# Performance work log

Hardware: AMD Instinct MI355X
Metric: run time of the kernel (lower is better)

The kernel has to match this reference:

```python
import jax, jax.numpy as jnp
import numpy as np

S, B, E, H, L = 256, 32, 300, 2400, 3


def setup_inputs() -> dict:
    key = jax.random.key(0)
    ks = jax.random.split(key, 8)
    sent = jax.random.normal(ks[0], (S, B, E), dtype=jnp.float32)
    sent_len = jax.random.randint(ks[1], (B,), 1, S + 1, dtype=jnp.int32)
    # QRNN per-layer linear: in_dim -> 3*H (Z, F, O gates), nn.Linear layout [3H, in]
    def lin(k, fan_in):
        s = 1.0 / np.sqrt(fan_in)
        kw, kb = jax.random.split(k)
        W = jax.random.uniform(kw, (3 * H, fan_in), jnp.float32, -s, s)
        b = jax.random.uniform(kb, (3 * H,), jnp.float32, -s, s)
        return W, b
    W1, b1 = lin(ks[2], E)
    W2, b2 = lin(ks[3], H)
    W3, b3 = lin(ks[4], H)
    return {"sent": sent, "sent_len": sent_len,
            "W1": W1, "b1": b1, "W2": W2, "b2": b2, "W3": W3, "b3": b3}


def _qrnn_layer(x, W, b):
    # x: [S, B, D] -> gates [S, B, 3H]
    Y = jnp.einsum('sbd,hd->sbh', x, W) + b
    Z, F, O = jnp.split(Y, 3, axis=-1)
    Z = jnp.tanh(Z)
    F = jax.nn.sigmoid(F)
    O = jax.nn.sigmoid(O)
    c0 = jnp.zeros(Z.shape[1:], Z.dtype)  # [B, H]
    def step(c, zf):
        z, f = zf
        c = f * c + (1.0 - f) * z  # fo-pool elementwise recurrence
        return c, c
    c_last, C = jax.lax.scan(step, c0, (Z, F))
    return O * C, c_last  # hidden seq [S,B,H], final cell [B,H]


def reference(sent, sent_len, W1, b1, W2, b2, W3, b3):
    x = sent
    finals = []
    for (W, b) in ((W1, b1), (W2, b2), (W3, b3)):
        x, c_last = _qrnn_layer(x, W, b)
        finals.append(c_last)
    hidden = jnp.stack(finals, axis=0)  # [L, B, H] == qrnn(...)[1]
    # mean pool as written in the module: sum over dim 0, divide by sent_len
    out = jnp.sum(hidden, axis=0) / sent_len.astype(jnp.float32)[:, None]
    return out  # [B, H]
```

## Files before the change

### kernel.cpp

```cpp
#include <hip/hip_runtime.h>
#include <math.h>
#include <stdint.h>
#include <stddef.h>

#define AS1 __attribute__((address_space(1)))
#define AS3 __attribute__((address_space(3)))

typedef __attribute__((ext_vector_type(8))) __bf16 bf16x8;
typedef __attribute__((ext_vector_type(4))) float f32x4;

#define SQ   256
#define BQ   32
#define EQ   300
#define HQ   2400
#define MQ   (SQ * BQ)
#define N3H  7200
#define N2H  4800
#define KP1  320
#define KP2  2432

__device__ __forceinline__ uint16_t f2bf(float x) {
    uint32_t u = __float_as_uint(x);
    u += 0x7FFFu + ((u >> 16) & 1u);
    return (uint16_t)(u >> 16);
}
__device__ __forceinline__ float bf2f(uint16_t b) {
    return __uint_as_float(((uint32_t)b) << 16);
}
__device__ __forceinline__ float sigm(float x) { return 1.f / (1.f + __expf(-x)); }

__global__ void conv_split(const float* __restrict__ src, uint16_t* __restrict__ hi,
                           uint16_t* __restrict__ lo, int rows, int K, int Kp) {
    int idx = blockIdx.x * 256 + threadIdx.x;
    int total = rows * Kp;
    if (idx >= total) return;
    int r = idx / Kp;
    int k = idx - r * Kp;
    float v = 0.f;
    if (k < K) v = src[(size_t)r * K + k];
    uint16_t h = f2bf(v);
    hi[idx] = h;
    lo[idx] = f2bf(v - bf2f(h));
}

__global__ void zero_pad_X(uint16_t* __restrict__ hi, uint16_t* __restrict__ lo) {
    int idx = blockIdx.x * 256 + threadIdx.x;
    if (idx >= MQ * (KP2 - HQ)) return;
    int r = idx >> 5;
    int c = idx & 31;
    size_t off = (size_t)r * KP2 + HQ + c;
    hi[off] = 0;
    lo[off] = 0;
}

__global__ __launch_bounds__(256, 2) void gemm_split(
    const uint16_t* __restrict__ Ahi, const uint16_t* __restrict__ Alo,
    const uint16_t* __restrict__ Whi, const uint16_t* __restrict__ Wlo,
    float* __restrict__ Y, int Kp, int Ncols, int rowbase)
{
    __shared__ uint16_t lds[4][128][64];
    const int tid  = threadIdx.x;
    const int lane = tid & 63;
    const int wave = tid >> 6;
    const int wm   = wave >> 1;
    const int wn   = wave & 1;
    const int lrow0 = blockIdx.y << 7;
    const int col0  = blockIdx.x << 7;

    const int sr = (wave << 3) + (lane >> 3);
    const int sk = (lane & 7) << 3;
    const int fr = lane & 15;
    const int fk = (lane >> 4) << 3;

    f32x4 acc[4][4];
    f32x4 zero = {0.f, 0.f, 0.f, 0.f};
#pragma unroll
    for (int i = 0; i < 4; ++i)
#pragma unroll
        for (int j = 0; j < 4; ++j) acc[i][j] = zero;

    char* ldsb = (char*)&lds[0][0][0];

    for (int k0 = 0; k0 < Kp; k0 += 64) {
#pragma unroll
        for (int i = 0; i < 4; ++i) {
            const int rr = (i << 5) + sr;
            const size_t ka = (size_t)(rowbase + lrow0 + rr) * Kp + (k0 + sk);
            const int wr = min(col0 + rr, Ncols - 1);
            const size_t kw = (size_t)wr * Kp + (k0 + sk);
            const int lofs = ((i << 5) + (wave << 3)) << 7;
            __builtin_amdgcn_global_load_lds((const AS1 uint32_t*)(Ahi + ka),
                                             (AS3 uint32_t*)(ldsb + lofs),         16, 0, 0);
            __builtin_amdgcn_global_load_lds((const AS1 uint32_t*)(Alo + ka),
                                             (AS3 uint32_t*)(ldsb + 16384 + lofs), 16, 0, 0);
            __builtin_amdgcn_global_load_lds((const AS1 uint32_t*)(Whi + kw),
                                             (AS3 uint32_t*)(ldsb + 32768 + lofs), 16, 0, 0);
            __builtin_amdgcn_global_load_lds((const AS1 uint32_t*)(Wlo + kw),
                                             (AS3 uint32_t*)(ldsb + 49152 + lofs), 16, 0, 0);
        }
        __syncthreads();

#pragma unroll
        for (int kk = 0; kk < 2; ++kk) {
            bf16x8 ah[4], al[4], bh[4], bl[4];
#pragma unroll
            for (int t = 0; t < 4; ++t) {
                ah[t] = *(const bf16x8*)&lds[0][(wm << 6) + (t << 4) + fr][(kk << 5) + fk];
                al[t] = *(const bf16x8*)&lds[1][(wm << 6) + (t << 4) + fr][(kk << 5) + fk];
                bh[t] = *(const bf16x8*)&lds[2][(wn << 6) + (t << 4) + fr][(kk << 5) + fk];
                bl[t] = *(const bf16x8*)&lds[3][(wn << 6) + (t << 4) + fr][(kk << 5) + fk];
            }
#pragma unroll
            for (int mi = 0; mi < 4; ++mi)
#pragma unroll
                for (int ni = 0; ni < 4; ++ni) {
                    acc[mi][ni] = __builtin_amdgcn_mfma_f32_16x16x32_bf16(ah[mi], bh[ni], acc[mi][ni], 0, 0, 0);
                    acc[mi][ni] = __builtin_amdgcn_mfma_f32_16x16x32_bf16(ah[mi], bl[ni], acc[mi][ni], 0, 0, 0);
                    acc[mi][ni] = __builtin_amdgcn_mfma_f32_16x16x32_bf16(al[mi], bh[ni], acc[mi][ni], 0, 0, 0);
                }
        }
        __syncthreads();
    }

    const int orow = (lane >> 4) << 2;
    const int ocol = lane & 15;
#pragma unroll
    for (int mi = 0; mi < 4; ++mi) {
        const int r0 = lrow0 + (wm << 6) + (mi << 4) + orow;
#pragma unroll
        for (int ni = 0; ni < 4; ++ni) {
            const int c = col0 + (wn << 6) + (ni << 4) + ocol;
            if (c < Ncols) {
                float* yp = Y + (size_t)r0 * Ncols + c;
#pragma unroll
                for (int r = 0; r < 4; ++r) yp[(size_t)r * Ncols] = acc[mi][ni][r];
            }
        }
    }
}

template<int MODE>
__global__ void scan_k(const float* __restrict__ Y, const float* __restrict__ bias,
                       uint16_t* __restrict__ hhi, uint16_t* __restrict__ hlo,
                       float* __restrict__ cst, float* __restrict__ fin,
                       float* __restrict__ out, const int* __restrict__ slen,
                       int s0, int Sc)
{
    int idx = blockIdx.x * 256 + threadIdx.x;
    if (idx >= BQ * HQ) return;
    int b = idx / HQ;
    int h = idx - b * HQ;
    const int Ncols = (MODE == 2) ? N2H : N3H;

    const float bz = bias[h], bfg = bias[HQ + h];
    const float bo = (MODE == 2) ? 0.f : bias[2 * HQ + h];
    float c = (s0 == 0) ? 0.f : cst[idx];
    const float* yp = Y + (size_t)b * Ncols + h;
    for (int si = 0; si < Sc; ++si) {
        const float* row = yp + (size_t)si * (BQ * Ncols);
        float z = tanhf(row[0] + bz);
        float f = sigm(row[HQ] + bfg);
        c = f * c + (1.f - f) * z;
        if (MODE != 2) {
            float o = sigm(row[2 * HQ] + bo);
            float hv = o * c;
            uint16_t hb = f2bf(hv);
            size_t off = ((size_t)(s0 + si) * BQ + b) * KP2 + h;
            hhi[off] = hb;
            hlo[off] = f2bf(hv - bf2f(hb));
        }
    }
    if (s0 + Sc < SQ) {
        cst[idx] = c;
    } else {
        if (MODE == 0)      fin[idx] = c;
        else if (MODE == 1) fin[idx] += c;
        else                out[idx] = (fin[idx] + c) / (float)slen[b];
    }
}

extern "C" void kernel_launch(void* const* d_in, const int* in_sizes, int n_in,
                              void* d_out, int out_size, void* d_ws, size_t ws_size,
                              hipStream_t stream) {
    const float* sent = (const float*)d_in[0];
    const int*   slen = (const int*)d_in[1];
    const float* Wl[3] = {(const float*)d_in[2], (const float*)d_in[4], (const float*)d_in[6]};
    const float* bl[3] = {(const float*)d_in[3], (const float*)d_in[5], (const float*)d_in[7]};
    float* out = (float*)d_out;

    char* ws = (char*)d_ws;
    uint16_t* A1hi = (uint16_t*)ws;
    uint16_t* A1lo = A1hi + (size_t)MQ * KP1;
    uint16_t* Xhi  = A1lo + (size_t)MQ * KP1;
    uint16_t* Xlo  = Xhi  + (size_t)MQ * KP2;
    uint16_t* Whi  = Xlo  + (size_t)MQ * KP2;
    uint16_t* Wlo  = Whi  + (size_t)N3H * KP2;
    float*    cst  = (float*)(Wlo + (size_t)N3H * KP2);
    float*    fin  = cst + (size_t)BQ * HQ;
    float*    Yc   = fin + (size_t)BQ * HQ;

    const size_t fixed = (size_t)((char*)Yc - ws);
    int Sc = 4;
    const int sc_opts[7] = {256, 128, 64, 32, 16, 8, 4};
    for (int i = 0; i < 7; ++i) {
        size_t need = fixed + (size_t)sc_opts[i] * BQ * N3H * 4 + 256;
        if (need <= ws_size) { Sc = sc_opts[i]; break; }
    }

    conv_split<<<(MQ * KP1 + 255) / 256, 256, 0, stream>>>(sent, A1hi, A1lo, MQ, EQ, KP1);
    zero_pad_X<<<(MQ * 32 + 255) / 256, 256, 0, stream>>>(Xhi, Xlo);

    const int sgrid = (BQ * HQ + 255) / 256;
    for (int l = 0; l < 3; ++l) {
        const int Ncols = (l == 2) ? N2H : N3H;
        const int Kp    = (l == 0) ? KP1 : KP2;
        const int Ksrc  = (l == 0) ? EQ  : HQ;
        conv_split<<<(Ncols * Kp + 255) / 256, 256, 0, stream>>>(Wl[l], Whi, Wlo, Ncols, Ksrc, Kp);
        const uint16_t* Ah = (l == 0) ? A1hi : Xhi;
        const uint16_t* Al = (l == 0) ? A1lo : Xlo;
        dim3 gg((Ncols + 127) / 128, Sc / 4);
        for (int s0 = 0; s0 < SQ; s0 += Sc) {
            gemm_split<<<gg, 256, 0, stream>>>(Ah, Al, Whi, Wlo, Yc, Kp, Ncols, s0 * BQ);
            if (l == 0)
                scan_k<0><<<sgrid, 256, 0, stream>>>(Yc, bl[0], Xhi, Xlo, cst, fin, nullptr, nullptr, s0, Sc);
            else if (l == 1)
                scan_k<1><<<sgrid, 256, 0, stream>>>(Yc, bl[1], Xhi, Xlo, cst, fin, nullptr, nullptr, s0, Sc);
            else
                scan_k<2><<<sgrid, 256, 0, stream>>>(Yc, bl[2], nullptr, nullptr, cst, fin, out, slen, s0, Sc);
        }
    }
}
```

Measured before the change: 2.623 ms.

## Replace split-bf16 GEMM with 256x256 pipelined 4-stage LDS kernel and vectorize helpers

The GEMM moves from 128x128 tiles with 256 threads to 256x256 tiles with 512 threads. It uses a 4-slot dynamic LDS ring buffer with XOR-swizzled layout and explicit vmcnt waits to overlap loads with MFMA. The three split-precision products (hi*hi, hi*lo, lo*hi) become separate K-slab segments rather than being interleaved per tile. The conversion, padding and scan kernels now process two elements per thread with packed stores, and tanh is replaced by an exp-based form. This aims to raise MFMA utilization and cut the global traffic per output, at the cost of 128KB LDS per block, which limits occupancy.

```diff
diff --git a/kernel.cpp b/kernel.cpp
--- a/kernel.cpp
+++ b/kernel.cpp
@@ -28,112 +28,143 @@
     return __uint_as_float(((uint32_t)b) << 16);
 }
 __device__ __forceinline__ float sigm(float x) { return 1.f / (1.f + __expf(-x)); }
+__device__ __forceinline__ float tanh_f(float x) { return 2.f / (1.f + __expf(-2.f * x)) - 1.f; }
 
 __global__ void conv_split(const float* __restrict__ src, uint16_t* __restrict__ hi,
                            uint16_t* __restrict__ lo, int rows, int K, int Kp) {
     int idx = blockIdx.x * 256 + threadIdx.x;
-    int total = rows * Kp;
-    if (idx >= total) return;
-    int r = idx / Kp;
-    int k = idx - r * Kp;
-    float v = 0.f;
-    if (k < K) v = src[(size_t)r * K + k];
-    uint16_t h = f2bf(v);
-    hi[idx] = h;
-    lo[idx] = f2bf(v - bf2f(h));
+    int kp2 = Kp >> 1;
+    if (idx >= rows * kp2) return;
+    int r = idx / kp2;
+    int k = (idx - r * kp2) << 1;
+    float2 v = make_float2(0.f, 0.f);
+    if (k < K) v = *(const float2*)(src + (size_t)r * K + k);
+    uint16_t h0 = f2bf(v.x), h1 = f2bf(v.y);
+    uint32_t hw = (uint32_t)h0 | ((uint32_t)h1 << 16);
+    uint32_t lw = (uint32_t)f2bf(v.x - bf2f(h0)) | ((uint32_t)f2bf(v.y - bf2f(h1)) << 16);
+    size_t o = (size_t)r * Kp + k;
+    *(uint32_t*)(hi + o) = hw;
+    *(uint32_t*)(lo + o) = lw;
 }
 
 __global__ void zero_pad_X(uint16_t* __restrict__ hi, uint16_t* __restrict__ lo) {
     int idx = blockIdx.x * 256 + threadIdx.x;
-    if (idx >= MQ * (KP2 - HQ)) return;
-    int r = idx >> 5;
-    int c = idx & 31;
+    if (idx >= MQ * ((KP2 - HQ) >> 1)) return;
+    int r = idx >> 4;
+    int c = (idx & 15) << 1;
     size_t off = (size_t)r * KP2 + HQ + c;
-    hi[off] = 0;
-    lo[off] = 0;
-}
-
-__global__ __launch_bounds__(256, 2) void gemm_split(
+    *(uint32_t*)(hi + off) = 0u;
+    *(uint32_t*)(lo + off) = 0u;
+}
+
+template<int KP>
+__global__ __launch_bounds__(512, 2) void gemm256(
     const uint16_t* __restrict__ Ahi, const uint16_t* __restrict__ Alo,
     const uint16_t* __restrict__ Whi, const uint16_t* __restrict__ Wlo,
-    float* __restrict__ Y, int Kp, int Ncols, int rowbase)
+    float* __restrict__ Y, int Ncols, int rowbase)
 {
-    __shared__ uint16_t lds[4][128][64];
+    constexpr int SPS   = KP / 32;
+    constexpr int NSLAB = 3 * SPS;
+    extern __shared__ char smem[];
+
     const int tid  = threadIdx.x;
     const int lane = tid & 63;
     const int wave = tid >> 6;
-    const int wm   = wave >> 1;
-    const int wn   = wave & 1;
-    const int lrow0 = blockIdx.y << 7;
-    const int col0  = blockIdx.x << 7;
-
-    const int sr = (wave << 3) + (lane >> 3);
-    const int sk = (lane & 7) << 3;
-    const int fr = lane & 15;
-    const int fk = (lane >> 4) << 3;
-
-    f32x4 acc[4][4];
-    f32x4 zero = {0.f, 0.f, 0.f, 0.f};
-#pragma unroll
-    for (int i = 0; i < 4; ++i)
-#pragma unroll
-        for (int j = 0; j < 4; ++j) acc[i][j] = zero;
-
-    char* ldsb = (char*)&lds[0][0][0];
-
-    for (int k0 = 0; k0 < Kp; k0 += 64) {
-#pragma unroll
-        for (int i = 0; i < 4; ++i) {
-            const int rr = (i << 5) + sr;
-            const size_t ka = (size_t)(rowbase + lrow0 + rr) * Kp + (k0 + sk);
-            const int wr = min(col0 + rr, Ncols - 1);
-            const size_t kw = (size_t)wr * Kp + (k0 + sk);
-            const int lofs = ((i << 5) + (wave << 3)) << 7;
-            __builtin_amdgcn_global_load_lds((const AS1 uint32_t*)(Ahi + ka),
-                                             (AS3 uint32_t*)(ldsb + lofs),         16, 0, 0);
-            __builtin_amdgcn_global_load_lds((const AS1 uint32_t*)(Alo + ka),
-                                             (AS3 uint32_t*)(ldsb + 16384 + lofs), 16, 0, 0);
-            __builtin_amdgcn_global_load_lds((const AS1 uint32_t*)(Whi + kw),
-                                             (AS3 uint32_t*)(ldsb + 32768 + lofs), 16, 0, 0);
-            __builtin_amdgcn_global_load_lds((const AS1 uint32_t*)(Wlo + kw),
-                                             (AS3 uint32_t*)(ldsb + 49152 + lofs), 16, 0, 0);
-        }
-        __syncthreads();
-
-#pragma unroll
-        for (int kk = 0; kk < 2; ++kk) {
-            bf16x8 ah[4], al[4], bh[4], bl[4];
-#pragma unroll
-            for (int t = 0; t < 4; ++t) {
-                ah[t] = *(const bf16x8*)&lds[0][(wm << 6) + (t << 4) + fr][(kk << 5) + fk];
-                al[t] = *(const bf16x8*)&lds[1][(wm << 6) + (t << 4) + fr][(kk << 5) + fk];
-                bh[t] = *(const bf16x8*)&lds[2][(wn << 6) + (t << 4) + fr][(kk << 5) + fk];
-                bl[t] = *(const bf16x8*)&lds[3][(wn << 6) + (t << 4) + fr][(kk << 5) + fk];
-            }
-#pragma unroll
-            for (int mi = 0; mi < 4; ++mi)
-#pragma unroll
-                for (int ni = 0; ni < 4; ++ni) {
-                    acc[mi][ni] = __builtin_amdgcn_mfma_f32_16x16x32_bf16(ah[mi], bh[ni], acc[mi][ni], 0, 0, 0);
-                    acc[mi][ni] = __builtin_amdgcn_mfma_f32_16x16x32_bf16(ah[mi], bl[ni], acc[mi][ni], 0, 0, 0);
-                    acc[mi][ni] = __builtin_amdgcn_mfma_f32_16x16x32_bf16(al[mi], bh[ni], acc[mi][ni], 0, 0, 0);
-                }
-        }
-        __syncthreads();
-    }
+    const int wm   = wave >> 2;
+    const int wn   = wave & 3;
+    const int lrow0 = blockIdx.y << 8;
+    const int col0  = blockIdx.x << 8;
+    const int arow0 = rowbase + lrow0;
+
+    const int tq    = tid >> 2;
+    const int c_log = (((tid & 3) << 4) ^ ((tq & 3) << 4));
+    const int k_el  = c_log >> 1;
+    const size_t aofs0 = (size_t)(arow0 + tq) * KP + k_el;
+    const size_t aofs1 = (size_t)(arow0 + 128 + tq) * KP + k_el;
+    const int wr0 = min(col0 + tq, Ncols - 1);
+    const int wr1 = min(col0 + 128 + tq, Ncols - 1);
+    const size_t bofs0 = (size_t)wr0 * KP + k_el;
+    const size_t bofs1 = (size_t)wr1 * KP + k_el;
+    const int ldst = tid << 4;
+
+    const int cphys = (((lane >> 4) << 4) ^ ((lane & 3) << 4));
+    const int abase = (((wm << 7) + (lane & 15)) << 6) + cphys;
+    const int bbase = (((wn << 6) + (lane & 15)) << 6) + cphys;
+
+    f32x4 acc[8][4];
+    {
+        f32x4 z = {0.f, 0.f, 0.f, 0.f};
+#pragma unroll
+        for (int mb = 0; mb < 8; ++mb)
+#pragma unroll
+            for (int nb = 0; nb < 4; ++nb) acc[mb][nb] = z;
+    }
+
+    int sseg = 0, sk0 = 0;
+    auto stage = [&](int slot) {
+        const uint16_t* Ab = (sseg == 2) ? Alo : Ahi;
+        const uint16_t* Bb = (sseg == 1) ? Wlo : Whi;
+        char* dst = smem + (slot << 15);
+        __builtin_amdgcn_global_load_lds((const AS1 uint32_t*)(Ab + aofs0 + sk0),
+                                         (AS3 uint32_t*)(dst + ldst),          16, 0, 0);
+        __builtin_amdgcn_global_load_lds((const AS1 uint32_t*)(Ab + aofs1 + sk0),
+                                         (AS3 uint32_t*)(dst + 8192  + ldst),  16, 0, 0);
+        __builtin_amdgcn_global_load_lds((const AS1 uint32_t*)(Bb + bofs0 + sk0),
+                                         (AS3 uint32_t*)(dst + 16384 + ldst),  16, 0, 0);
+        __builtin_amdgcn_global_load_lds((const AS1 uint32_t*)(Bb + bofs1 + sk0),
+                                         (AS3 uint32_t*)(dst + 24576 + ldst),  16, 0, 0);
+        sk0 += 32;
+        if (sk0 == KP) { sk0 = 0; ++sseg; }
+    };
+
+    auto compute = [&](int slot) {
+        const char* sa = smem + (slot << 15);
+        const char* sb = sa + 16384;
+        bf16x8 af[8], bfr[4];
+#pragma unroll
+        for (int mb = 0; mb < 8; ++mb) af[mb] = *(const bf16x8*)(sa + abase + (mb << 10));
+#pragma unroll
+        for (int nb = 0; nb < 4; ++nb) bfr[nb] = *(const bf16x8*)(sb + bbase + (nb << 10));
+        __builtin_amdgcn_s_setprio(1);
+#pragma unroll
+        for (int mb = 0; mb < 8; ++mb)
+#pragma unroll
+            for (int nb = 0; nb < 4; ++nb)
+                acc[mb][nb] = __builtin_amdgcn_mfma_f32_16x16x32_bf16(af[mb], bfr[nb], acc[mb][nb], 0, 0, 0);
+        __builtin_amdgcn_s_setprio(0);
+    };
+
+    stage(0); stage(1); stage(2);
+
+    for (int j = 0; j < NSLAB - 3; ++j) {
+        stage((j + 3) & 3);
+        asm volatile("s_waitcnt vmcnt(12)" ::: "memory");
+        asm volatile("s_barrier" ::: "memory");
+        compute(j & 3);
+        asm volatile("s_barrier" ::: "memory");
+    }
+    asm volatile("s_waitcnt vmcnt(8)" ::: "memory");
+    asm volatile("s_barrier" ::: "memory");
+    compute((NSLAB - 3) & 3);
+    asm volatile("s_waitcnt vmcnt(4)" ::: "memory");
+    asm volatile("s_barrier" ::: "memory");
+    compute((NSLAB - 2) & 3);
+    asm volatile("s_waitcnt vmcnt(0)" ::: "memory");
+    asm volatile("s_barrier" ::: "memory");
+    compute((NSLAB - 1) & 3);
 
     const int orow = (lane >> 4) << 2;
     const int ocol = lane & 15;
 #pragma unroll
-    for (int mi = 0; mi < 4; ++mi) {
-        const int r0 = lrow0 + (wm << 6) + (mi << 4) + orow;
-#pragma unroll
-        for (int ni = 0; ni < 4; ++ni) {
-            const int c = col0 + (wn << 6) + (ni << 4) + ocol;
+    for (int mb = 0; mb < 8; ++mb) {
+        const int r0 = lrow0 + (wm << 7) + (mb << 4) + orow;
+#pragma unroll
+        for (int nb = 0; nb < 4; ++nb) {
+            const int c = col0 + (wn << 6) + (nb << 4) + ocol;
             if (c < Ncols) {
                 float* yp = Y + (size_t)r0 * Ncols + c;
 #pragma unroll
-                for (int r = 0; r < 4; ++r) yp[(size_t)r * Ncols] = acc[mi][ni][r];
+                for (int r = 0; r < 4; ++r) yp[(size_t)r * Ncols] = acc[mb][nb][r];
             }
         }
     }
@@ -147,35 +178,51 @@
                        int s0, int Sc)
 {
     int idx = blockIdx.x * 256 + threadIdx.x;
-    if (idx >= BQ * HQ) return;
-    int b = idx / HQ;
-    int h = idx - b * HQ;
+    if (idx >= BQ * (HQ >> 1)) return;
+    int b = idx / (HQ >> 1);
+    int h = (idx - b * (HQ >> 1)) << 1;
     const int Ncols = (MODE == 2) ? N2H : N3H;
 
-    const float bz = bias[h], bfg = bias[HQ + h];
-    const float bo = (MODE == 2) ? 0.f : bias[2 * HQ + h];
-    float c = (s0 == 0) ? 0.f : cst[idx];
+    const float2 bz = *(const float2*)(bias + h);
+    const float2 bg = *(const float2*)(bias + HQ + h);
+    const float2 bo = (MODE == 2) ? make_float2(0.f, 0.f) : *(const float2*)(bias + 2 * HQ + h);
+    float2 c = (s0 == 0) ? make_float2(0.f, 0.f) : *(const float2*)(cst + b * HQ + h);
+
     const float* yp = Y + (size_t)b * Ncols + h;
     for (int si = 0; si < Sc; ++si) {
         const float* row = yp + (size_t)si * (BQ * Ncols);
-        float z = tanhf(row[0] + bz);
-        float f = sigm(row[HQ] + bfg);
-        c = f * c + (1.f - f) * z;
+        float2 zr = *(const float2*)(row);
+        float2 fr = *(const float2*)(row + HQ);
+        float z0 = tanh_f(zr.x + bz.x), z1 = tanh_f(zr.y + bz.y);
+        float f0 = sigm(fr.x + bg.x),   f1 = sigm(fr.y + bg.y);
+        c.x = f0 * c.x + (1.f - f0) * z0;
+        c.y = f1 * c.y + (1.f - f1) * z1;
         if (MODE != 2) {
-            float o = sigm(row[2 * HQ] + bo);
-            float hv = o * c;
-            uint16_t hb = f2bf(hv);
+            float2 orv = *(const float2*)(row + 2 * HQ);
+            float o0 = sigm(orv.x + bo.x), o1 = sigm(orv.y + bo.y);
+            float h0 = o0 * c.x, h1 = o1 * c.y;
+            uint16_t hb0 = f2bf(h0), hb1 = f2bf(h1);
             size_t off = ((size_t)(s0 + si) * BQ + b) * KP2 + h;
-            hhi[off] = hb;
-            hlo[off] = f2bf(hv - bf2f(hb));
+            *(uint32_t*)(hhi + off) = (uint32_t)hb0 | ((uint32_t)hb1 << 16);
+            *(uint32_t*)(hlo + off) =
+                (uint32_t)f2bf(h0 - bf2f(hb0)) | ((uint32_t)f2bf(h1 - bf2f(hb1)) << 16);
         }
     }
     if (s0 + Sc < SQ) {
-        cst[idx] = c;
+        *(float2*)(cst + b * HQ + h) = c;
     } else {
-        if (MODE == 0)      fin[idx] = c;
-        else if (MODE == 1) fin[idx] += c;
-        else                out[idx] = (fin[idx] + c) / (float)slen[b];
+        if (MODE == 0) {
+            *(float2*)(fin + b * HQ + h) = c;
+        } else if (MODE == 1) {
+            float2 t = *(const float2*)(fin + b * HQ + h);
+            t.x += c.x; t.y += c.y;
+            *(float2*)(fin + b * HQ + h) = t;
+        } else {
+            float inv = 1.f / (float)slen[b];
+            float2 t = *(const float2*)(fin + b * HQ + h);
+            out[b * HQ + h]     = (t.x + c.x) * inv;
+            out[b * HQ + h + 1] = (t.y + c.y) * inv;
+        }
     }
 }
 
@@ -187,6 +234,11 @@
     const float* Wl[3] = {(const float*)d_in[2], (const float*)d_in[4], (const float*)d_in[6]};
     const float* bl[3] = {(const float*)d_in[3], (const float*)d_in[5], (const float*)d_in[7]};
     float* out = (float*)d_out;
+
+    (void)hipFuncSetAttribute((const void*)gemm256<KP1>,
+                              hipFuncAttributeMaxDynamicSharedMemorySize, 131072);
+    (void)hipFuncSetAttribute((const void*)gemm256<KP2>,
+                              hipFuncAttributeMaxDynamicSharedMemorySize, 131072);
 
     char* ws = (char*)d_ws;
     uint16_t* A1hi = (uint16_t*)ws;
@@ -200,27 +252,30 @@
     float*    Yc   = fin + (size_t)BQ * HQ;
 
     const size_t fixed = (size_t)((char*)Yc - ws);
-    int Sc = 4;
-    const int sc_opts[7] = {256, 128, 64, 32, 16, 8, 4};
-    for (int i = 0; i < 7; ++i) {
+    int Sc = 8;
+    const int sc_opts[6] = {256, 128, 64, 32, 16, 8};
+    for (int i = 0; i < 6; ++i) {
         size_t need = fixed + (size_t)sc_opts[i] * BQ * N3H * 4 + 256;
         if (need <= ws_size) { Sc = sc_opts[i]; break; }
     }
 
-    conv_split<<<(MQ * KP1 + 255) / 256, 256, 0, stream>>>(sent, A1hi, A1lo, MQ, EQ, KP1);
-    zero_pad_X<<<(MQ * 32 + 255) / 256, 256, 0, stream>>>(Xhi, Xlo);
-
-    const int sgrid = (BQ * HQ + 255) / 256;
+    conv_split<<<(MQ * (KP1 / 2) + 255) / 256, 256, 0, stream>>>(sent, A1hi, A1lo, MQ, EQ, KP1);
+    zero_pad_X<<<(MQ * 16 + 255) / 256, 256, 0, stream>>>(Xhi, Xlo);
+
+    const int sgrid = (BQ * (HQ / 2) + 255) / 256;
     for (int l = 0; l < 3; ++l) {
         const int Ncols = (l == 2) ? N2H : N3H;
         const int Kp    = (l == 0) ? KP1 : KP2;
         const int Ksrc  = (l == 0) ? EQ  : HQ;
-        conv_split<<<(Ncols * Kp + 255) / 256, 256, 0, stream>>>(Wl[l], Whi, Wlo, Ncols, Ksrc, Kp);
+        conv_split<<<(Ncols * (Kp / 2) + 255) / 256, 256, 0, stream>>>(Wl[l], Whi, Wlo, Ncols, Ksrc, Kp);
         const uint16_t* Ah = (l == 0) ? A1hi : Xhi;
         const uint16_t* Al = (l == 0) ? A1lo : Xlo;
-        dim3 gg((Ncols + 127) / 128, Sc / 4);
+        dim3 gg((Ncols + 255) / 256, Sc / 8);
         for (int s0 = 0; s0 < SQ; s0 += Sc) {
-            gemm_split<<<gg, 256, 0, stream>>>(Ah, Al, Whi, Wlo, Yc, Kp, Ncols, s0 * BQ);
+            if (l == 0)
+                gemm256<KP1><<<gg, 512, 131072, stream>>>(Ah, Al, Whi, Wlo, Yc, Ncols, s0 * BQ);
+            else
+                gemm256<KP2><<<gg, 512, 131072, stream>>>(Ah, Al, Whi, Wlo, Yc, Ncols, s0 * BQ);
             if (l == 0)
                 scan_k<0><<<sgrid, 256, 0, stream>>>(Yc, bl[0], Xhi, Xlo, cst, fin, nullptr, nullptr, s0, Sc);
             else if (l == 1)
```

Measured after the change: 2.630 ms. No clear change (+0.3%).
